# Performance work log

Measured on AMD Instinct MI355X. Metric: run time of the kernel, lower is better.

The kernel has to match this reference:

```python
import jax, jax.numpy as jnp
import numpy as np

SCALE = 8.0  # sqrt(head_dim=64)
B, H, S, D = 2, 16, 2048, 64


def setup_inputs() -> dict:
    key = jax.random.key(0)
    kq, kk, kv = jax.random.split(key, 3)
    query = jax.random.normal(kq, (B, H, S, D), dtype=jnp.float32)
    key_t = jax.random.normal(kk, (B, H, S, D), dtype=jnp.float32)
    value = jax.random.normal(kv, (B, H, S, D), dtype=jnp.float32)
    # causal target mask (B, 1, S, S); 0 = masked
    mask = jnp.broadcast_to(jnp.tril(jnp.ones((S, S), dtype=jnp.int32)), (B, 1, S, S))
    return {"query": query, "key": key_t, "value": value, "mask": mask}


def reference(query, key, value, mask):
    # scores: (B, H, S, S)
    scores = jnp.einsum("bhqd,bhkd->bhqk", query, key) / SCALE
    scores = jnp.where(mask == 0, -jnp.inf, scores)
    attn = jax.nn.softmax(scores, axis=-1)  # dropout_rate=0.0 -> identity
    return jnp.einsum("bhqk,bhkd->bhqd", attn, value)
```

## Files before the change

kernel.cpp:

```cpp
#include <hip/hip_runtime.h>
#include <hip/hip_bf16.h>


#define S_ 2048
#define D_ 64
#define NBH 32

typedef __bf16 bf16x8 __attribute__((ext_vector_type(8)));
typedef float f32x16 __attribute__((ext_vector_type(16)));
typedef unsigned short u16x4 __attribute__((ext_vector_type(4)));
typedef unsigned short u16x8 __attribute__((ext_vector_type(8)));
typedef unsigned int u32;
typedef u32 u32x4 __attribute__((ext_vector_type(4)));

static __device__ __forceinline__ unsigned short bfb(float f) {
    return __builtin_bit_cast(unsigned short, (__bf16)f);
}
static __device__ __forceinline__ u32 pk2(float lo, float hi) {
    return (u32)bfb(lo) | ((u32)bfb(hi) << 16);
}

__global__ __launch_bounds__(256)
void prep_kv(const float* __restrict__ K, const float* __restrict__ V,
             unsigned short* __restrict__ Kbf, unsigned short* __restrict__ Vt) {
    const int bh = blockIdx.x >> 5;
    const int kvbase = (blockIdx.x & 31) << 6;

    const float* Ks = K + (size_t)bh * S_ * D_ + (size_t)kvbase * D_;
    unsigned short* Kd = Kbf + (size_t)bh * S_ * D_ + (size_t)kvbase * D_;
    #pragma unroll
    for (int i = 0; i < 4; ++i) {
        const int p = i * 256 + threadIdx.x;
        float4 x = reinterpret_cast<const float4*>(Ks)[p];
        u16x4 o = { bfb(x.x), bfb(x.y), bfb(x.z), bfb(x.w) };
        reinterpret_cast<u16x4*>(Kd)[p] = o;
    }

    __shared__ float Vl[64][65];
    const float* Vb = V + (size_t)bh * S_ * D_ + (size_t)kvbase * D_;
    #pragma unroll
    for (int i = 0; i < 4; ++i) {
        const int flat = i * 1024 + threadIdx.x * 4;
        const int kv = flat >> 6, d = flat & 63;
        float4 x = *reinterpret_cast<const float4*>(Vb + kv * D_ + d);
        Vl[kv][d] = x.x; Vl[kv][d + 1] = x.y; Vl[kv][d + 2] = x.z; Vl[kv][d + 3] = x.w;
    }
    __syncthreads();
    unsigned short* Vo = Vt + (size_t)bh * D_ * S_;
    #pragma unroll
    for (int i = 0; i < 2; ++i) {
        const int p = i * 256 + threadIdx.x;
        const int d = p >> 3, c = p & 7;
        u16x8 o;
        #pragma unroll
        for (int j = 0; j < 8; ++j) o[j] = bfb(Vl[c * 8 + j][d]);
        *reinterpret_cast<u16x8*>(Vo + d * S_ + kvbase + c * 8) = o;
    }
}

#define MFMA32(a, b, c) __builtin_amdgcn_mfma_f32_32x32x16_bf16((a), (b), (c), 0, 0, 0)

__global__ __launch_bounds__(128, 2)
void attn_fwd4(const float* __restrict__ Q, const unsigned short* __restrict__ Kbf,
               const unsigned short* __restrict__ Vtbf, float* __restrict__ O) {
    const int tid  = threadIdx.x;
    const int wq   = tid >> 6;
    const int lane = tid & 63;
    const int lq   = lane & 31;
    const int hi   = lane >> 5;

    const int bid = blockIdx.x;
    const int qb  = 31 - (bid >> 5);
    const int bh  = bid & 31;
    const int q0  = qb * 64 + wq * 32;

    const unsigned short* Kg = Kbf  + (size_t)bh * S_ * D_;
    const unsigned short* Vg = Vtbf + (size_t)bh * D_ * S_;

    __shared__ __align__(16) unsigned short Kl[2][4096];
    __shared__ __align__(16) unsigned short Vl[2][4096];

    const float qscale = 0.18033688011112042f;
    bf16x8 qf[4];
    {
        const float* qsrc = Q + ((size_t)bh * S_ + q0 + lq) * D_;
        #pragma unroll
        for (int ks = 0; ks < 4; ++ks) {
            const float* p = qsrc + ks * 16 + hi * 8;
            float4 x = *reinterpret_cast<const float4*>(p);
            float4 y = *reinterpret_cast<const float4*>(p + 4);
            union { unsigned short u[8]; bf16x8 v; } t;
            t.u[0] = bfb(x.x * qscale); t.u[1] = bfb(x.y * qscale);
            t.u[2] = bfb(x.z * qscale); t.u[3] = bfb(x.w * qscale);
            t.u[4] = bfb(y.x * qscale); t.u[5] = bfb(y.y * qscale);
            t.u[6] = bfb(y.z * qscale); t.u[7] = bfb(y.w * qscale);
            qf[ks] = t.v;
        }
    }

    const unsigned short* kSrc[4];
    const unsigned short* vSrc[4];
    #pragma unroll
    for (int j = 0; j < 4; ++j) {
        const int p = j * 128 + tid, row = p >> 3;
        const int sc = (p & 7) ^ (row & 7);
        kSrc[j] = Kg + row * 64 + sc * 8;
        vSrc[j] = Vg + (size_t)row * S_ + sc * 8;
    }
    auto stage = [&](int buf, int t) {
        #pragma unroll
        for (int j = 0; j < 4; ++j) {
            const int p = j * 128 + tid;
            __builtin_amdgcn_global_load_lds(
                (const __attribute__((address_space(1))) void*)(kSrc[j] + t * 4096),
                (__attribute__((address_space(3))) void*)&Kl[buf][p * 8], 16, 0, 0);
            __builtin_amdgcn_global_load_lds(
                (const __attribute__((address_space(1))) void*)(vSrc[j] + t * 64),
                (__attribute__((address_space(3))) void*)&Vl[buf][p * 8], 16, 0, 0);
        }
    };

    f32x16 oa0, oa1;
    #pragma unroll
    for (int r = 0; r < 16; ++r) { oa0[r] = 0.f; oa1[r] = 0.f; }
    float m_ = -__builtin_inff(), l_ = 0.f;

    const int nkv = qb + 1;
    stage(0, 0);
    __syncthreads();

    for (int t = 0; t < nkv; ++t) {
        if (t + 1 < nkv) stage((t + 1) & 1, t + 1);
        const unsigned short* Kb_ = Kl[t & 1];
        const unsigned short* Vb_ = Vl[t & 1];

        f32x16 s0, s1;
        #pragma unroll
        for (int r = 0; r < 16; ++r) { s0[r] = 0.f; s1[r] = 0.f; }
        __builtin_amdgcn_s_setprio(1);
        #pragma unroll
        for (int ks = 0; ks < 4; ++ks) {
            const int cc = 2 * ks + hi;
            bf16x8 k0 = *reinterpret_cast<const bf16x8*>(
                &Kb_[((lq)*8      + (cc ^ (lq & 7))) * 8]);
            bf16x8 k1 = *reinterpret_cast<const bf16x8*>(
                &Kb_[((32 + lq)*8 + (cc ^ (lq & 7))) * 8]);
            s0 = MFMA32(k0, qf[ks], s0);
            s1 = MFMA32(k1, qf[ks], s1);
        }
        __builtin_amdgcn_s_setprio(0);

        if (t == nkv - 1) {
            const int qg = q0 + lq - t * 64;
            #pragma unroll
            for (int r = 0; r < 16; ++r) {
                const int kv0 = (r & 3) + 8 * (r >> 2) + 4 * hi;
                if (kv0 > qg)      s0[r] = -__builtin_inff();
                if (kv0 + 32 > qg) s1[r] = -__builtin_inff();
            }
        }

        float v = s0[0];
        #pragma unroll
        for (int r = 1; r < 16; ++r) v = fmaxf(v, s0[r]);
        #pragma unroll
        for (int r = 0; r < 16; ++r) v = fmaxf(v, s1[r]);
        v = fmaxf(v, __shfl_xor(v, 32));

        if (__any(v > m_ + 8.0f ? 1 : 0)) {
            const float mn = fmaxf(m_, v);
            const float al = __builtin_amdgcn_exp2f(m_ - mn);
            m_ = mn;
            l_ *= al;
            #pragma unroll
            for (int r = 0; r < 16; ++r) { oa0[r] *= al; oa1[r] *= al; }
        }
        #pragma unroll
        for (int r = 0; r < 16; ++r) {
            s0[r] = __builtin_amdgcn_exp2f(s0[r] - m_);
            s1[r] = __builtin_amdgcn_exp2f(s1[r] - m_);
        }
        {
            float rs = 0.f;
            #pragma unroll
            for (int r = 0; r < 16; ++r) rs += s0[r] + s1[r];
            rs += __shfl_xor(rs, 32);
            l_ += rs;
        }

        u32 c0[4][2], c1[4][2];
        #pragma unroll
        for (int tq = 0; tq < 4; ++tq) {
            c0[tq][0] = pk2(s0[4*tq+0], s0[4*tq+1]);
            c0[tq][1] = pk2(s0[4*tq+2], s0[4*tq+3]);
            c1[tq][0] = pk2(s1[4*tq+0], s1[4*tq+1]);
            c1[tq][1] = pk2(s1[4*tq+2], s1[4*tq+3]);
        }

        __builtin_amdgcn_s_setprio(1);
#define PVSTEP(KS, C) { \
            const int tl = (2*(KS)) & 3; \
            u32 a0 = C[tl][0], a1 = C[tl][1], b0 = C[tl+1][0], b1 = C[tl+1][1]; \
            u32 pa0 = __shfl_xor(a0, 32), pa1 = __shfl_xor(a1, 32); \
            u32 pb0 = __shfl_xor(b0, 32), pb1 = __shfl_xor(b1, 32); \
            u32x4 w = { hi ? pb0 : a0, hi ? pb1 : a1, hi ? b0 : pa0, hi ? b1 : pa1 }; \
            bf16x8 pf = __builtin_bit_cast(bf16x8, w); \
            const int cc = 2*(KS) + hi; \
            bf16x8 v0 = *reinterpret_cast<const bf16x8*>( \
                &Vb_[((lq)*8      + (cc ^ (lq & 7))) * 8]); \
            bf16x8 v1 = *reinterpret_cast<const bf16x8*>( \
                &Vb_[((32 + lq)*8 + (cc ^ (lq & 7))) * 8]); \
            oa0 = MFMA32(v0, pf, oa0); \
            oa1 = MFMA32(v1, pf, oa1); }
        PVSTEP(0, c0) PVSTEP(1, c0) PVSTEP(2, c1) PVSTEP(3, c1)
#undef PVSTEP
        __builtin_amdgcn_s_setprio(0);

        __syncthreads();
    }

    const float inv = 1.0f / l_;
    float* Ob = O + ((size_t)bh * S_ + q0 + lq) * D_;
    #pragma unroll
    for (int g = 0; g < 4; ++g) {
        float4 o0 = { oa0[4*g+0]*inv, oa0[4*g+1]*inv, oa0[4*g+2]*inv, oa0[4*g+3]*inv };
        *reinterpret_cast<float4*>(&Ob[8*g + 4*hi]) = o0;
        float4 o1 = { oa1[4*g+0]*inv, oa1[4*g+1]*inv, oa1[4*g+2]*inv, oa1[4*g+3]*inv };
        *reinterpret_cast<float4*>(&Ob[32 + 8*g + 4*hi]) = o1;
    }
}

extern "C" void kernel_launch(void* const* d_in, const int* in_sizes, int n_in,
                              void* d_out, int out_size, void* d_ws, size_t ws_size,
                              hipStream_t stream) {
    const float* Q = (const float*)d_in[0];
    const float* K = (const float*)d_in[1];
    const float* V = (const float*)d_in[2];
    float* O = (float*)d_out;

    unsigned short* Kbf = (unsigned short*)d_ws;
    unsigned short* Vt  = Kbf + (size_t)NBH * S_ * D_;

    hipLaunchKernelGGL(prep_kv,   dim3(1024), dim3(256), 0, stream, K, V, Kbf, Vt);
    hipLaunchKernelGGL(attn_fwd4, dim3(1024), dim3(128), 0, stream, Q, Kbf, Vt, O);
}
```

Measured before the change: 153.9 us.

## Widen attention blocks to 128 queries, MFMA row sums, permlane swap

Each block now covers 128 query rows with 4 waves that share staged K/V tiles, so the grid halves and each K/V tile is loaded once for twice as many queries. Waves past their causal limit skip compute but still join the barriers. The softmax row sum is now accumulated by an extra MFMA against a ones vector instead of a scalar add plus shuffle. The cross-half P exchange uses v_permlane32_swap instead of four shuffles and selects. The extra MFMA per step and the idle waves on the diagonal tile add cost, and the grid of 512 blocks gives less scheduling slack.

```diff
diff --git a/kernel.cpp b/kernel.cpp
--- a/kernel.cpp
+++ b/kernel.cpp
@@ -60,8 +60,8 @@
 
 #define MFMA32(a, b, c) __builtin_amdgcn_mfma_f32_32x32x16_bf16((a), (b), (c), 0, 0, 0)
 
-__global__ __launch_bounds__(128, 2)
-void attn_fwd4(const float* __restrict__ Q, const unsigned short* __restrict__ Kbf,
+__global__ __launch_bounds__(256, 2)
+void attn_fwd6(const float* __restrict__ Q, const unsigned short* __restrict__ Kbf,
                const unsigned short* __restrict__ Vtbf, float* __restrict__ O) {
     const int tid  = threadIdx.x;
     const int wq   = tid >> 6;
@@ -70,9 +70,12 @@
     const int hi   = lane >> 5;
 
     const int bid = blockIdx.x;
-    const int qb  = 31 - (bid >> 5);
     const int bh  = bid & 31;
-    const int q0  = qb * 64 + wq * 32;
+    const int jb  = 15 - (bid >> 5);
+    const int q0w = jb * 128 + wq * 32;
+
+    const int nkv_b = 2 * jb + 2;
+    const int nkv_w = 2 * jb + 1 + (wq >> 1);
 
     const unsigned short* Kg = Kbf  + (size_t)bh * S_ * D_;
     const unsigned short* Vg = Vtbf + (size_t)bh * D_ * S_;
@@ -83,7 +86,7 @@
     const float qscale = 0.18033688011112042f;
     bf16x8 qf[4];
     {
-        const float* qsrc = Q + ((size_t)bh * S_ + q0 + lq) * D_;
+        const float* qsrc = Q + ((size_t)bh * S_ + q0w + lq) * D_;
         #pragma unroll
         for (int ks = 0; ks < 4; ++ks) {
             const float* p = qsrc + ks * 16 + hi * 8;
@@ -98,112 +101,108 @@
         }
     }
 
-    const unsigned short* kSrc[4];
-    const unsigned short* vSrc[4];
-    #pragma unroll
-    for (int j = 0; j < 4; ++j) {
-        const int p = j * 128 + tid, row = p >> 3;
+    bf16x8 ones;
+    #pragma unroll
+    for (int i = 0; i < 8; ++i) ones[i] = (__bf16)1.0f;
+
+    const unsigned short* kSrc[2];
+    const unsigned short* vSrc[2];
+    #pragma unroll
+    for (int i = 0; i < 2; ++i) {
+        const int p = i * 256 + tid, row = p >> 3;
         const int sc = (p & 7) ^ (row & 7);
-        kSrc[j] = Kg + row * 64 + sc * 8;
-        vSrc[j] = Vg + (size_t)row * S_ + sc * 8;
+        kSrc[i] = Kg + row * 64 + sc * 8;
+        vSrc[i] = Vg + (size_t)row * S_ + sc * 8;
     }
     auto stage = [&](int buf, int t) {
         #pragma unroll
-        for (int j = 0; j < 4; ++j) {
-            const int p = j * 128 + tid;
+        for (int i = 0; i < 2; ++i) {
+            const int p = i * 256 + tid;
             __builtin_amdgcn_global_load_lds(
-                (const __attribute__((address_space(1))) void*)(kSrc[j] + t * 4096),
+                (const __attribute__((address_space(1))) void*)(kSrc[i] + t * 4096),
                 (__attribute__((address_space(3))) void*)&Kl[buf][p * 8], 16, 0, 0);
             __builtin_amdgcn_global_load_lds(
-                (const __attribute__((address_space(1))) void*)(vSrc[j] + t * 64),
+                (const __attribute__((address_space(1))) void*)(vSrc[i] + t * 64),
                 (__attribute__((address_space(3))) void*)&Vl[buf][p * 8], 16, 0, 0);
         }
     };
 
-    f32x16 oa0, oa1;
-    #pragma unroll
-    for (int r = 0; r < 16; ++r) { oa0[r] = 0.f; oa1[r] = 0.f; }
-    float m_ = -__builtin_inff(), l_ = 0.f;
-
-    const int nkv = qb + 1;
+    f32x16 oa0, oa1, ssum;
+    #pragma unroll
+    for (int r = 0; r < 16; ++r) { oa0[r] = 0.f; oa1[r] = 0.f; ssum[r] = 0.f; }
+    float m_ = -__builtin_inff();
+
     stage(0, 0);
     __syncthreads();
 
-    for (int t = 0; t < nkv; ++t) {
-        if (t + 1 < nkv) stage((t + 1) & 1, t + 1);
-        const unsigned short* Kb_ = Kl[t & 1];
-        const unsigned short* Vb_ = Vl[t & 1];
-
-        f32x16 s0, s1;
-        #pragma unroll
-        for (int r = 0; r < 16; ++r) { s0[r] = 0.f; s1[r] = 0.f; }
-        __builtin_amdgcn_s_setprio(1);
-        #pragma unroll
-        for (int ks = 0; ks < 4; ++ks) {
-            const int cc = 2 * ks + hi;
-            bf16x8 k0 = *reinterpret_cast<const bf16x8*>(
-                &Kb_[((lq)*8      + (cc ^ (lq & 7))) * 8]);
-            bf16x8 k1 = *reinterpret_cast<const bf16x8*>(
-                &Kb_[((32 + lq)*8 + (cc ^ (lq & 7))) * 8]);
-            s0 = MFMA32(k0, qf[ks], s0);
-            s1 = MFMA32(k1, qf[ks], s1);
-        }
-        __builtin_amdgcn_s_setprio(0);
-
-        if (t == nkv - 1) {
-            const int qg = q0 + lq - t * 64;
+    for (int t = 0; t < nkv_b; ++t) {
+        if (t + 1 < nkv_b) stage((t + 1) & 1, t + 1);
+        if (t < nkv_w) {
+            const unsigned short* Kb_ = Kl[t & 1];
+            const unsigned short* Vb_ = Vl[t & 1];
+
+            f32x16 s0, s1;
+            #pragma unroll
+            for (int r = 0; r < 16; ++r) { s0[r] = 0.f; s1[r] = 0.f; }
+            __builtin_amdgcn_s_setprio(1);
+            #pragma unroll
+            for (int ks = 0; ks < 4; ++ks) {
+                const int cc = 2 * ks + hi;
+                bf16x8 k0 = *reinterpret_cast<const bf16x8*>(
+                    &Kb_[((lq)*8      + (cc ^ (lq & 7))) * 8]);
+                bf16x8 k1 = *reinterpret_cast<const bf16x8*>(
+                    &Kb_[((32 + lq)*8 + (cc ^ (lq & 7))) * 8]);
+                s0 = MFMA32(k0, qf[ks], s0);
+                s1 = MFMA32(k1, qf[ks], s1);
+            }
+            __builtin_amdgcn_s_setprio(0);
+
+            if (t == nkv_w - 1) {
+                const int qg = q0w + lq - t * 64;
+                #pragma unroll
+                for (int r = 0; r < 16; ++r) {
+                    const int kv0 = (r & 3) + 8 * (r >> 2) + 4 * hi;
+                    if (kv0 > qg)      s0[r] = -__builtin_inff();
+                    if (kv0 + 32 > qg) s1[r] = -__builtin_inff();
+                }
+            }
+
+            float v = s0[0];
+            #pragma unroll
+            for (int r = 1; r < 16; ++r) v = fmaxf(v, s0[r]);
+            #pragma unroll
+            for (int r = 0; r < 16; ++r) v = fmaxf(v, s1[r]);
+            v = fmaxf(v, __shfl_xor(v, 32));
+
+            if (__any(v > m_ + 8.0f ? 1 : 0)) {
+                const float mn = fmaxf(m_, v);
+                const float al = __builtin_amdgcn_exp2f(m_ - mn);
+                m_ = mn;
+                ssum[0] *= al;
+                #pragma unroll
+                for (int r = 0; r < 16; ++r) { oa0[r] *= al; oa1[r] *= al; }
+            }
             #pragma unroll
             for (int r = 0; r < 16; ++r) {
-                const int kv0 = (r & 3) + 8 * (r >> 2) + 4 * hi;
-                if (kv0 > qg)      s0[r] = -__builtin_inff();
-                if (kv0 + 32 > qg) s1[r] = -__builtin_inff();
-            }
-        }
-
-        float v = s0[0];
-        #pragma unroll
-        for (int r = 1; r < 16; ++r) v = fmaxf(v, s0[r]);
-        #pragma unroll
-        for (int r = 0; r < 16; ++r) v = fmaxf(v, s1[r]);
-        v = fmaxf(v, __shfl_xor(v, 32));
-
-        if (__any(v > m_ + 8.0f ? 1 : 0)) {
-            const float mn = fmaxf(m_, v);
-            const float al = __builtin_amdgcn_exp2f(m_ - mn);
-            m_ = mn;
-            l_ *= al;
-            #pragma unroll
-            for (int r = 0; r < 16; ++r) { oa0[r] *= al; oa1[r] *= al; }
-        }
-        #pragma unroll
-        for (int r = 0; r < 16; ++r) {
-            s0[r] = __builtin_amdgcn_exp2f(s0[r] - m_);
-            s1[r] = __builtin_amdgcn_exp2f(s1[r] - m_);
-        }
-        {
-            float rs = 0.f;
-            #pragma unroll
-            for (int r = 0; r < 16; ++r) rs += s0[r] + s1[r];
-            rs += __shfl_xor(rs, 32);
-            l_ += rs;
-        }
-
-        u32 c0[4][2], c1[4][2];
-        #pragma unroll
-        for (int tq = 0; tq < 4; ++tq) {
-            c0[tq][0] = pk2(s0[4*tq+0], s0[4*tq+1]);
-            c0[tq][1] = pk2(s0[4*tq+2], s0[4*tq+3]);
-            c1[tq][0] = pk2(s1[4*tq+0], s1[4*tq+1]);
-            c1[tq][1] = pk2(s1[4*tq+2], s1[4*tq+3]);
-        }
-
-        __builtin_amdgcn_s_setprio(1);
-#define PVSTEP(KS, C) { \
-            const int tl = (2*(KS)) & 3; \
-            u32 a0 = C[tl][0], a1 = C[tl][1], b0 = C[tl+1][0], b1 = C[tl+1][1]; \
-            u32 pa0 = __shfl_xor(a0, 32), pa1 = __shfl_xor(a1, 32); \
-            u32 pb0 = __shfl_xor(b0, 32), pb1 = __shfl_xor(b1, 32); \
-            u32x4 w = { hi ? pb0 : a0, hi ? pb1 : a1, hi ? b0 : pa0, hi ? b1 : pa1 }; \
+                s0[r] = __builtin_amdgcn_exp2f(s0[r] - m_);
+                s1[r] = __builtin_amdgcn_exp2f(s1[r] - m_);
+            }
+
+            u32 c0[4][2], c1[4][2];
+            #pragma unroll
+            for (int tq = 0; tq < 4; ++tq) {
+                c0[tq][0] = pk2(s0[4*tq+0], s0[4*tq+1]);
+                c0[tq][1] = pk2(s0[4*tq+2], s0[4*tq+3]);
+                c1[tq][0] = pk2(s1[4*tq+0], s1[4*tq+1]);
+                c1[tq][1] = pk2(s1[4*tq+2], s1[4*tq+3]);
+            }
+
+            __builtin_amdgcn_s_setprio(1);
+#define PVSTEP(KS, C, TL) { \
+            u32 a0 = C[TL][0], a1 = C[TL][1], b0 = C[TL+1][0], b1 = C[TL+1][1]; \
+            asm volatile("v_permlane32_swap_b32 %0, %1" : "+v"(a0), "+v"(b0)); \
+            asm volatile("v_permlane32_swap_b32 %0, %1" : "+v"(a1), "+v"(b1)); \
+            u32x4 w = { a0, a1, b0, b1 }; \
             bf16x8 pf = __builtin_bit_cast(bf16x8, w); \
             const int cc = 2*(KS) + hi; \
             bf16x8 v0 = *reinterpret_cast<const bf16x8*>( \
@@ -211,16 +210,17 @@
             bf16x8 v1 = *reinterpret_cast<const bf16x8*>( \
                 &Vb_[((32 + lq)*8 + (cc ^ (lq & 7))) * 8]); \
             oa0 = MFMA32(v0, pf, oa0); \
-            oa1 = MFMA32(v1, pf, oa1); }
-        PVSTEP(0, c0) PVSTEP(1, c0) PVSTEP(2, c1) PVSTEP(3, c1)
+            oa1 = MFMA32(v1, pf, oa1); \
+            ssum = MFMA32(ones, pf, ssum); }
+            PVSTEP(0, c0, 0) PVSTEP(1, c0, 2) PVSTEP(2, c1, 0) PVSTEP(3, c1, 2)
 #undef PVSTEP
-        __builtin_amdgcn_s_setprio(0);
-
+            __builtin_amdgcn_s_setprio(0);
+        }
         __syncthreads();
     }
 
-    const float inv = 1.0f / l_;
-    float* Ob = O + ((size_t)bh * S_ + q0 + lq) * D_;
+    const float inv = 1.0f / ssum[0];
+    float* Ob = O + ((size_t)bh * S_ + q0w + lq) * D_;
     #pragma unroll
     for (int g = 0; g < 4; ++g) {
         float4 o0 = { oa0[4*g+0]*inv, oa0[4*g+1]*inv, oa0[4*g+2]*inv, oa0[4*g+3]*inv };
@@ -242,5 +242,5 @@
     unsigned short* Vt  = Kbf + (size_t)NBH * S_ * D_;
 
     hipLaunchKernelGGL(prep_kv,   dim3(1024), dim3(256), 0, stream, K, V, Kbf, Vt);
-    hipLaunchKernelGGL(attn_fwd4, dim3(1024), dim3(128), 0, stream, Q, Kbf, Vt, O);
-}
+    hipLaunchKernelGGL(attn_fwd6, dim3(512),  dim3(256), 0, stream, Q, Kbf, Vt, O);
+}
```

Result: no change. 152.5 us (-1.0%).
